# Optimization experiments

Hardware: AMD Instinct MI355X
Metric: run time of the kernel (lower is better)

The kernel has to match this reference:

```python
import jax, jax.numpy as jnp
import numpy as np

INPUT_SIZE = 1024
MODULE_SIZE = 256   # k
N_MODULES = 8       # g
HIDDEN = MODULE_SIZE * N_MODULES
T = 4096
PERIODS = jnp.array([2 ** i for i in range(N_MODULES)], dtype=jnp.int32)  # [1,2,...,128]


def setup_inputs() -> dict:
    key = jax.random.key(0)
    k1, k2, k3, k4, k5 = jax.random.split(key, 5)
    s = 1.0 / np.sqrt(HIDDEN)
    return {
        "x": jax.random.normal(k1, (T, INPUT_SIZE), dtype=jnp.float32),
        "W_ih": jax.random.normal(k2, (HIDDEN, INPUT_SIZE), dtype=jnp.float32) * s,
        "W_hh": jax.random.normal(k3, (HIDDEN, HIDDEN), dtype=jnp.float32) * s,
        "b_ih": jax.random.normal(k4, (HIDDEN,), dtype=jnp.float32) * s,
        "b_hh": jax.random.normal(k5, (HIDDEN,), dtype=jnp.float32) * s,
    }


def reference(x, W_ih, W_hh, b_ih, b_hh):
    # Clockwork RNN: at step t (1-indexed, curr_t starts at 1 for hx=None),
    # module j is active iff t % period_j == 0. Masking the weight columns
    # (rows of W^T) is equivalent to masking the pre-activation output, and
    # tanh(0)=0 so inactive modules keep their previous hidden value.
    ts = jnp.arange(1, x.shape[0] + 1, dtype=jnp.int32)

    def step(h, inp):
        xt, t = inp  # xt: (input_size,), t: scalar int
        mask = jnp.repeat((t % PERIODS) == 0, MODULE_SIZE).astype(h.dtype)  # (H,)
        pre = xt @ W_ih.T + b_ih + h @ W_hh.T + b_hh                        # (H,)
        h_new = h * (1.0 - mask) + jnp.tanh(pre * mask)
        return h_new, h_new

    h0 = jnp.zeros((HIDDEN,), dtype=x.dtype)
    _, outs = jax.lax.scan(step, h0, (x, ts))
    return outs  # (T, HIDDEN)
```

## Files before the change

### kernel.cpp

```cpp
#include <hip/hip_runtime.h>
#include <math.h>

#define T_STEPS 4096
#define HID     2048
#define MOD     256
#define INSZ    1024
#define NB_REC  16
#define TPB_REC 1024
#define WPB     (TPB_REC / 64)

static __device__ __forceinline__ unsigned long long agent_load_u64(
        const unsigned long long* p) {
    return __hip_atomic_load((unsigned long long*)p, __ATOMIC_RELAXED,
                             __HIP_MEMORY_SCOPE_AGENT);
}
static __device__ __forceinline__ void agent_store_u64(
        unsigned long long* p, unsigned long long v) {
    __hip_atomic_store(p, v, __ATOMIC_RELAXED, __HIP_MEMORY_SCOPE_AGENT);
}

#define BM 128
#define BN 128
#define BK 8

__global__ __launch_bounds__(256) void gemm_u(
    const float* __restrict__ x, const float* __restrict__ Wih,
    const float* __restrict__ bih, const float* __restrict__ bhh,
    float* __restrict__ out)
{
    __shared__ float As[BK][BM];
    __shared__ float Bs[BK][BN];

    const int tid = threadIdx.x;
    const int t0 = blockIdx.y * BM;
    const int i0 = blockIdx.x * BN;
    const int tx = tid & 15;
    const int ty = tid >> 4;
    const int arow = tid >> 1;
    const int acol = (tid & 1) * 4;

    float acc[8][8];
#pragma unroll
    for (int a = 0; a < 8; ++a)
#pragma unroll
        for (int b = 0; b < 8; ++b) acc[a][b] = 0.0f;

    for (int k0 = 0; k0 < INSZ; k0 += BK) {
        float4 av = *(const float4*)(x   + (size_t)(t0 + arow) * INSZ + k0 + acol);
        float4 bv = *(const float4*)(Wih + (size_t)(i0 + arow) * INSZ + k0 + acol);
        __syncthreads();
        As[acol + 0][arow] = av.x; As[acol + 1][arow] = av.y;
        As[acol + 2][arow] = av.z; As[acol + 3][arow] = av.w;
        Bs[acol + 0][arow] = bv.x; Bs[acol + 1][arow] = bv.y;
        Bs[acol + 2][arow] = bv.z; Bs[acol + 3][arow] = bv.w;
        __syncthreads();
#pragma unroll
        for (int kk = 0; kk < BK; ++kk) {
            float a[8], b[8];
            *(float4*)&a[0] = *(const float4*)&As[kk][ty * 8];
            *(float4*)&a[4] = *(const float4*)&As[kk][ty * 8 + 4];
            *(float4*)&b[0] = *(const float4*)&Bs[kk][tx * 8];
            *(float4*)&b[4] = *(const float4*)&Bs[kk][tx * 8 + 4];
#pragma unroll
            for (int ri = 0; ri < 8; ++ri)
#pragma unroll
                for (int ci = 0; ci < 8; ++ci)
                    acc[ri][ci] = fmaf(a[ri], b[ci], acc[ri][ci]);
        }
    }

    float bias[8];
#pragma unroll
    for (int ci = 0; ci < 8; ++ci) {
        int i = i0 + tx * 8 + ci;
        bias[ci] = bih[i] + bhh[i];
    }
#pragma unroll
    for (int ri = 0; ri < 8; ++ri) {
        int t = t0 + ty * 8 + ri;
#pragma unroll
        for (int ci = 0; ci < 8; ++ci) {
            int i = i0 + tx * 8 + ci;
            out[(size_t)t * HID + i] = acc[ri][ci] + bias[ci];
        }
    }
}

__global__ __launch_bounds__(TPB_REC) void cwrnn_rec(
    float* __restrict__ out, const float* __restrict__ Whh,
    unsigned long long* __restrict__ comm)
{
    __shared__ float hs[HID];
    const int tid   = threadIdx.x;
    const int lane  = tid & 63;
    const int wid   = tid >> 6;
    const int gwave = blockIdx.x * WPB + wid;

    float4 w0[8];
    {
        const float4* wr = (const float4*)(Whh + (size_t)gwave * HID);
#pragma unroll
        for (int j = 0; j < 8; ++j) w0[j] = wr[lane + 64 * j];
    }

    for (int k = tid; k < HID; k += TPB_REC) hs[k] = 0.0f;

    int Rprev = HID;
    for (int t = 1; t <= T_STEPS; ++t) {
        if (t > 1) {
            float* prow = out + (size_t)(t - 2) * HID;
            for (int k = Rprev + blockIdx.x * TPB_REC + tid; k < HID;
                 k += NB_REC * TPB_REC)
                prow[k] = hs[k];

            const unsigned long long* csrc = comm + (size_t)((t - 1) & 1) * HID;
            const unsigned need = (unsigned)(t - 1);
            for (int k = tid; k < Rprev; k += TPB_REC) {
                unsigned long long v = agent_load_u64(csrc + k);
                while ((unsigned)(v >> 32) < need)
                    v = agent_load_u64(csrc + k);
                hs[k] = __uint_as_float((unsigned)v);
            }
        }
        __syncthreads();

        const int A = (__builtin_ctz(t) + 1 > 8) ? 8 : (__builtin_ctz(t) + 1);
        const int R = A * MOD;
        float* orow = out + (size_t)(t - 1) * HID;
        const float4* h4 = (const float4*)hs;
        unsigned long long* cdst = comm + (size_t)(t & 1) * HID;
        const unsigned long long tagbits = ((unsigned long long)(unsigned)t) << 32;

        float upf = 0.0f;
        if (lane < A) upf = orow[lane * MOD + gwave];

        {
            float acc = 0.0f;
#pragma unroll
            for (int j = 0; j < 8; ++j) {
                float4 h = h4[lane + 64 * j];
                acc = fmaf(w0[j].x, h.x, fmaf(w0[j].y, h.y,
                      fmaf(w0[j].z, h.z, fmaf(w0[j].w, h.w, acc))));
            }
#pragma unroll
            for (int off = 32; off; off >>= 1) acc += __shfl_xor(acc, off, 64);
            float u0 = __shfl(upf, 0, 64);
            if (lane == 0) {
                float hv = tanhf(u0 + acc);
                agent_store_u64(cdst + gwave,
                    tagbits | (unsigned long long)__float_as_uint(hv));
                orow[gwave] = hv;
            }
        }

        int m = 1;
        for (; m + 1 < A; m += 2) {
            const int ra = m * MOD + gwave;
            const int rb = ra + MOD;
            const float4* wa = (const float4*)(Whh + (size_t)ra * HID);
            const float4* wb = (const float4*)(Whh + (size_t)rb * HID);
            float acca = 0.0f, accb = 0.0f;
#pragma unroll
            for (int j = 0; j < 8; ++j) {
                float4 h = h4[lane + 64 * j];
                float4 a = wa[lane + 64 * j];
                float4 b = wb[lane + 64 * j];
                acca = fmaf(a.x, h.x, fmaf(a.y, h.y,
                       fmaf(a.z, h.z, fmaf(a.w, h.w, acca))));
                accb = fmaf(b.x, h.x, fmaf(b.y, h.y,
                       fmaf(b.z, h.z, fmaf(b.w, h.w, accb))));
            }
#pragma unroll
            for (int off = 32; off; off >>= 1) {
                acca += __shfl_xor(acca, off, 64);
                accb += __shfl_xor(accb, off, 64);
            }
            float ua = __shfl(upf, m, 64);
            float ub = __shfl(upf, m + 1, 64);
            if (lane == 0) {
                float hva = tanhf(ua + acca);
                float hvb = tanhf(ub + accb);
                agent_store_u64(cdst + ra,
                    tagbits | (unsigned long long)__float_as_uint(hva));
                agent_store_u64(cdst + rb,
                    tagbits | (unsigned long long)__float_as_uint(hvb));
                orow[ra] = hva;
                orow[rb] = hvb;
            }
        }
        if (m < A) {
            const int r = m * MOD + gwave;
            const float4* wr = (const float4*)(Whh + (size_t)r * HID);
            float acc = 0.0f;
#pragma unroll
            for (int j = 0; j < 8; ++j) {
                float4 h = h4[lane + 64 * j];
                float4 a = wr[lane + 64 * j];
                acc = fmaf(a.x, h.x, fmaf(a.y, h.y,
                      fmaf(a.z, h.z, fmaf(a.w, h.w, acc))));
            }
#pragma unroll
            for (int off = 32; off; off >>= 1) acc += __shfl_xor(acc, off, 64);
            float um = __shfl(upf, m, 64);
            if (lane == 0) {
                float hv = tanhf(um + acc);
                agent_store_u64(cdst + r,
                    tagbits | (unsigned long long)__float_as_uint(hv));
                orow[r] = hv;
            }
        }

        __syncthreads();
        Rprev = R;
    }

    {
        float* prow = out + (size_t)(T_STEPS - 1) * HID;
        for (int k = Rprev + blockIdx.x * TPB_REC + tid; k < HID;
             k += NB_REC * TPB_REC)
            prow[k] = hs[k];
    }
}

extern "C" void kernel_launch(void* const* d_in, const int* in_sizes, int n_in,
                              void* d_out, int out_size, void* d_ws, size_t ws_size,
                              hipStream_t stream) {
    const float* x   = (const float*)d_in[0];
    const float* Wih = (const float*)d_in[1];
    const float* Whh = (const float*)d_in[2];
    const float* bih = (const float*)d_in[3];
    const float* bhh = (const float*)d_in[4];
    float* out = (float*)d_out;
    unsigned long long* comm = (unsigned long long*)d_ws;

    hipMemsetAsync(d_ws, 0, 2 * HID * sizeof(unsigned long long), stream);

    dim3 g1(HID / BN, T_STEPS / BM);
    gemm_u<<<g1, 256, 0, stream>>>(x, Wih, bih, bhh, out);
    cwrnn_rec<<<NB_REC, TPB_REC, 0, stream>>>(out, Whh, comm);
}
```

Measured before the change: 13.85 ms.

## Use single-wave blocks holding hidden state in registers, removing block barriers

```diff
diff --git a/kernel.cpp b/kernel.cpp
--- a/kernel.cpp
+++ b/kernel.cpp
@@ -5,9 +5,7 @@
 #define HID     2048
 #define MOD     256
 #define INSZ    1024
-#define NB_REC  16
-#define TPB_REC 1024
-#define WPB     (TPB_REC / 64)
+#define NWAVE   256
 
 static __device__ __forceinline__ unsigned long long agent_load_u64(
         const unsigned long long* p) {
@@ -86,90 +84,118 @@
     }
 }
 
-__global__ __launch_bounds__(TPB_REC) void cwrnn_rec(
+__global__ __launch_bounds__(64, 1) void cwrnn_rec(
     float* __restrict__ out, const float* __restrict__ Whh,
     unsigned long long* __restrict__ comm)
 {
-    __shared__ float hs[HID];
-    const int tid   = threadIdx.x;
-    const int lane  = tid & 63;
-    const int wid   = tid >> 6;
-    const int gwave = blockIdx.x * WPB + wid;
+    const int lane = threadIdx.x;
+    const int g    = blockIdx.x;
+
+    float4 hreg[8];
+#pragma unroll
+    for (int j = 0; j < 8; ++j) hreg[j] = make_float4(0.f, 0.f, 0.f, 0.f);
 
     float4 w0[8];
     {
-        const float4* wr = (const float4*)(Whh + (size_t)gwave * HID);
+        const float4* wr = (const float4*)(Whh + (size_t)g * HID);
 #pragma unroll
         for (int j = 0; j < 8; ++j) w0[j] = wr[lane + 64 * j];
     }
 
-    for (int k = tid; k < HID; k += TPB_REC) hs[k] = 0.0f;
-
-    int Rprev = HID;
     for (int t = 1; t <= T_STEPS; ++t) {
+        const int ctz = __builtin_ctz(t);
+        const int A = (ctz + 1 > 8) ? 8 : (ctz + 1);
+        float* orow = out + (size_t)(t - 1) * HID;
+
+        float upf = (lane < A) ? orow[lane * MOD + g] : 0.0f;
+
         if (t > 1) {
-            float* prow = out + (size_t)(t - 2) * HID;
-            for (int k = Rprev + blockIdx.x * TPB_REC + tid; k < HID;
-                 k += NB_REC * TPB_REC)
-                prow[k] = hs[k];
-
-            const unsigned long long* csrc = comm + (size_t)((t - 1) & 1) * HID;
+            const int ctzp = __builtin_ctz(t - 1);
+            const int Ap = (ctzp + 1 > 8) ? 8 : (ctzp + 1);
             const unsigned need = (unsigned)(t - 1);
-            for (int k = tid; k < Rprev; k += TPB_REC) {
-                unsigned long long v = agent_load_u64(csrc + k);
-                while ((unsigned)(v >> 32) < need)
-                    v = agent_load_u64(csrc + k);
-                hs[k] = __uint_as_float((unsigned)v);
-            }
-        }
-        __syncthreads();
-
-        const int A = (__builtin_ctz(t) + 1 > 8) ? 8 : (__builtin_ctz(t) + 1);
-        const int R = A * MOD;
-        float* orow = out + (size_t)(t - 1) * HID;
-        const float4* h4 = (const float4*)hs;
+            const unsigned long long* csrc =
+                comm + (size_t)((t - 1) & 1) * HID + 4 * lane;
+            unsigned long long pv[8][4];
+            for (;;) {
+#pragma unroll
+                for (int j = 0; j < 8; ++j) {
+                    if (j < Ap) {
+                        pv[j][0] = agent_load_u64(csrc + j * MOD + 0);
+                        pv[j][1] = agent_load_u64(csrc + j * MOD + 1);
+                        pv[j][2] = agent_load_u64(csrc + j * MOD + 2);
+                        pv[j][3] = agent_load_u64(csrc + j * MOD + 3);
+                    }
+                }
+                bool ok = true;
+#pragma unroll
+                for (int j = 0; j < 8; ++j) {
+                    if (j < Ap)
+                        ok = ok && ((unsigned)(pv[j][0] >> 32) >= need)
+                                && ((unsigned)(pv[j][1] >> 32) >= need)
+                                && ((unsigned)(pv[j][2] >> 32) >= need)
+                                && ((unsigned)(pv[j][3] >> 32) >= need);
+                }
+                if (ok) break;
+            }
+#pragma unroll
+            for (int j = 0; j < 8; ++j) {
+                if (j < Ap)
+                    hreg[j] = make_float4(
+                        __uint_as_float((unsigned)pv[j][0]),
+                        __uint_as_float((unsigned)pv[j][1]),
+                        __uint_as_float((unsigned)pv[j][2]),
+                        __uint_as_float((unsigned)pv[j][3]));
+            }
+        }
+
         unsigned long long* cdst = comm + (size_t)(t & 1) * HID;
-        const unsigned long long tagbits = ((unsigned long long)(unsigned)t) << 32;
-
-        float upf = 0.0f;
-        if (lane < A) upf = orow[lane * MOD + gwave];
+        const unsigned long long tagbits =
+            ((unsigned long long)(unsigned)t) << 32;
 
         {
-            float acc = 0.0f;
-#pragma unroll
-            for (int j = 0; j < 8; ++j) {
-                float4 h = h4[lane + 64 * j];
-                acc = fmaf(w0[j].x, h.x, fmaf(w0[j].y, h.y,
-                      fmaf(w0[j].z, h.z, fmaf(w0[j].w, h.w, acc))));
-            }
+            float4 s = make_float4(0.f, 0.f, 0.f, 0.f);
+#pragma unroll
+            for (int j = 0; j < 8; ++j) {
+                s.x = fmaf(w0[j].x, hreg[j].x, s.x);
+                s.y = fmaf(w0[j].y, hreg[j].y, s.y);
+                s.z = fmaf(w0[j].z, hreg[j].z, s.z);
+                s.w = fmaf(w0[j].w, hreg[j].w, s.w);
+            }
+            float acc = (s.x + s.y) + (s.z + s.w);
 #pragma unroll
             for (int off = 32; off; off >>= 1) acc += __shfl_xor(acc, off, 64);
             float u0 = __shfl(upf, 0, 64);
             if (lane == 0) {
                 float hv = tanhf(u0 + acc);
-                agent_store_u64(cdst + gwave,
+                agent_store_u64(cdst + g,
                     tagbits | (unsigned long long)__float_as_uint(hv));
-                orow[gwave] = hv;
+                orow[g] = hv;
             }
         }
 
         int m = 1;
         for (; m + 1 < A; m += 2) {
-            const int ra = m * MOD + gwave;
+            const int ra = m * MOD + g;
             const int rb = ra + MOD;
             const float4* wa = (const float4*)(Whh + (size_t)ra * HID);
             const float4* wb = (const float4*)(Whh + (size_t)rb * HID);
-            float acca = 0.0f, accb = 0.0f;
-#pragma unroll
-            for (int j = 0; j < 8; ++j) {
-                float4 h = h4[lane + 64 * j];
+            float4 sa = make_float4(0.f, 0.f, 0.f, 0.f);
+            float4 sb = make_float4(0.f, 0.f, 0.f, 0.f);
+#pragma unroll
+            for (int j = 0; j < 8; ++j) {
                 float4 a = wa[lane + 64 * j];
                 float4 b = wb[lane + 64 * j];
-                acca = fmaf(a.x, h.x, fmaf(a.y, h.y,
-                       fmaf(a.z, h.z, fmaf(a.w, h.w, acca))));
-                accb = fmaf(b.x, h.x, fmaf(b.y, h.y,
-                       fmaf(b.z, h.z, fmaf(b.w, h.w, accb))));
-            }
+                sa.x = fmaf(a.x, hreg[j].x, sa.x);
+                sa.y = fmaf(a.y, hreg[j].y, sa.y);
+                sa.z = fmaf(a.z, hreg[j].z, sa.z);
+                sa.w = fmaf(a.w, hreg[j].w, sa.w);
+                sb.x = fmaf(b.x, hreg[j].x, sb.x);
+                sb.y = fmaf(b.y, hreg[j].y, sb.y);
+                sb.z = fmaf(b.z, hreg[j].z, sb.z);
+                sb.w = fmaf(b.w, hreg[j].w, sb.w);
+            }
+            float acca = (sa.x + sa.y) + (sa.z + sa.w);
+            float accb = (sb.x + sb.y) + (sb.z + sb.w);
 #pragma unroll
             for (int off = 32; off; off >>= 1) {
                 acca += __shfl_xor(acca, off, 64);
@@ -189,16 +215,18 @@
             }
         }
         if (m < A) {
-            const int r = m * MOD + gwave;
+            const int r = m * MOD + g;
             const float4* wr = (const float4*)(Whh + (size_t)r * HID);
-            float acc = 0.0f;
-#pragma unroll
-            for (int j = 0; j < 8; ++j) {
-                float4 h = h4[lane + 64 * j];
+            float4 s = make_float4(0.f, 0.f, 0.f, 0.f);
+#pragma unroll
+            for (int j = 0; j < 8; ++j) {
                 float4 a = wr[lane + 64 * j];
-                acc = fmaf(a.x, h.x, fmaf(a.y, h.y,
-                      fmaf(a.z, h.z, fmaf(a.w, h.w, acc))));
-            }
+                s.x = fmaf(a.x, hreg[j].x, s.x);
+                s.y = fmaf(a.y, hreg[j].y, s.y);
+                s.z = fmaf(a.z, hreg[j].z, s.z);
+                s.w = fmaf(a.w, hreg[j].w, s.w);
+            }
+            float acc = (s.x + s.y) + (s.z + s.w);
 #pragma unroll
             for (int off = 32; off; off >>= 1) acc += __shfl_xor(acc, off, 64);
             float um = __shfl(upf, m, 64);
@@ -210,15 +238,12 @@
             }
         }
 
-        __syncthreads();
-        Rprev = R;
-    }
-
-    {
-        float* prow = out + (size_t)(T_STEPS - 1) * HID;
-        for (int k = Rprev + blockIdx.x * TPB_REC + tid; k < HID;
-             k += NB_REC * TPB_REC)
-            prow[k] = hs[k];
+#pragma unroll
+        for (int j = 0; j < 8; ++j) {
+            if (j >= A && g == (j - A)) {
+                *(float4*)(orow + j * MOD + 4 * lane) = hreg[j];
+            }
+        }
     }
 }
 
@@ -237,5 +262,5 @@
 
     dim3 g1(HID / BN, T_STEPS / BM);
     gemm_u<<<g1, 256, 0, stream>>>(x, Wih, bih, bhh, out);
-    cwrnn_rec<<<NB_REC, TPB_REC, 0, stream>>>(out, Whh, comm);
-}
+    cwrnn_rec<<<NWAVE, 64, 0, stream>>>(out, Whh, comm);
+}
```

After: 11.20 ms. 1.24x faster.
